# Kernel optimization log

Hardware: AMD Instinct MI355X
Metric: run time of the kernel (lower is better)

The kernel has to match this reference:

```python
import jax, jax.numpy as jnp
import numpy as np

C = 768; H = 12; D = C // H; R = 8; SCALE = 0.5; EPS = 1e-12
NEG = -1e9

def _lin(x, W, b):
    return x @ W + b

def _ln(x, g, b):
    m = jnp.mean(x, axis=-1, keepdims=True)
    v = jnp.mean((x - m) ** 2, axis=-1, keepdims=True)
    return (x - m) * jax.lax.rsqrt(v + EPS) * g + b

def setup_inputs() -> dict:
    key = jax.random.key(0)
    ks = jax.random.split(key, 16)
    B, T, K = 8, 512, 4
    s = 0.02
    inp = {
        'x': jax.random.normal(ks[0], (B, T, C), jnp.float32),
        'mask': jnp.ones((B, T), jnp.int32),
        'neighbour_rep': jax.random.normal(ks[1], (B, T - 1, K, C), jnp.float32),
        'Wq': jax.random.normal(ks[2], (C, C), jnp.float32) * s,
        'bq': jnp.zeros((C,), jnp.float32),
        'Wk': jax.random.normal(ks[3], (C, C), jnp.float32) * s,
        'bk': jnp.zeros((C,), jnp.float32),
        'Wv': jax.random.normal(ks[4], (C, C), jnp.float32) * s,
        'bv': jnp.zeros((C,), jnp.float32),
        'Wp': jax.random.normal(ks[5], (C, C), jnp.float32) * s,
        'bp': jnp.zeros((C,), jnp.float32),
        'Wd': jax.random.normal(ks[6], (C, R), jnp.float32) * s,
        'bd': jnp.zeros((R,), jnp.float32),
        'Wu': jax.random.normal(ks[7], (R, C), jnp.float32) * s,
        'bu': jnp.zeros((C,), jnp.float32),
        'ln_g': jnp.ones((C,), jnp.float32),
        'ln_b': jnp.zeros((C,), jnp.float32),
    }
    return inp

def _softmax_stable(att):
    # manual max-sub-exp-sum softmax, matching stable_softmax
    att = att - jnp.max(att, axis=-1, keepdims=True)
    att = jnp.exp(att)
    return att / jnp.sum(att, axis=-1, keepdims=True)

def _heads(t, n_tok):
    B = t.shape[0]
    return t.reshape(B, n_tok, H, D)

def reference(x, mask, neighbour_rep, Wq, bq, Wk, bk, Wv, bv, Wp, bp, Wd, bd, Wu, bu, ln_g, ln_b):
    B, T, _ = x.shape
    inv = 1.0 / jnp.sqrt(jnp.float32(D))
    mvalid = (mask != 0)[:, None, None, :]  # [B,1,1,T]

    # ---- self attention: queries are x[:,1:], keys/values over full seq ----
    q = _heads(_lin(x[:, 1:], Wq, bq), T - 1)      # [B,T-1,H,D]
    k = _heads(_lin(x, Wk, bk), T)                 # [B,T,H,D]
    v = _heads(_lin(x, Wv, bv), T)
    att = jnp.einsum('bqhd,bkhd->bhqk', q, k) * inv
    att = jnp.where(mvalid, att, NEG)
    att = _softmax_stable(att)
    y_self = jnp.einsum('bhqk,bkhd->bqhd', att, v).reshape(B, T - 1, C)
    y_self = _lin(y_self, Wp, bp)

    # ---- cls attention: single query (token 0), low-rank key projection ----
    qc = _heads(_lin(x[:, :1], Wq, bq), 1)                         # [B,1,H,D]
    kc = _heads(_lin(_lin(x, Wd, bd), Wu, bu), T)                  # [B,T,H,D]
    attc = jnp.einsum('bqhd,bkhd->bhqk', qc, kc) * inv
    attc = jnp.where(mvalid, attc, NEG)
    attc = _softmax_stable(attc)
    y_cls = jnp.einsum('bhqk,bkhd->bqhd', attc, v).reshape(B, 1, C)
    y_cls = _lin(y_cls, Wp, bp)

    # ---- neighbour attention over small candidate set per token ----
    cand = jnp.concatenate([x[:, 1:, None, :], neighbour_rep], axis=2)  # [B,T-1,Kc,C]
    Kc = cand.shape[2]
    qn = _lin(cand, Wq, bq).reshape(B, T - 1, Kc, H, D)
    kn = _lin(_lin(cand, Wd, bd), Wu, bu).reshape(B, T - 1, Kc, H, D)
    vn = _lin(cand, Wv, bv).reshape(B, T - 1, Kc, H, D)
    attn = jnp.einsum('btihd,btjhd->bthij', qn, kn) * inv
    attn = _softmax_stable(attn)
    out = jnp.einsum('bthij,btjhd->btihd', attn, vn).reshape(B, T - 1, Kc, C)
    out = _lin(out, Wp, bp)
    y_neigh = out[:, :, 0, :]
    neigh_tmp = out[:, :, 1:, :]

    y = SCALE * y_neigh + (1.0 - SCALE) * y_self
    neighbour_out = _ln(neigh_tmp + neighbour_rep, ln_g, ln_b)
    y = jnp.concatenate([y_cls, y], axis=1)
    y = _ln(y + x, ln_g, ln_b)
    return y, neighbour_out
```

## Files before the change

### kernel.cpp

```cpp
#include <hip/hip_runtime.h>
#include <math.h>

#define C_    768
#define H_    12
#define D_    64
#define B_    8
#define T_    512
#define TM1   511
#define R_    8
#define KN_   4
#define KC5   5
#define SCALE_ 0.5f
#define EPS_  1e-12f
#define NEG_  -1000000000.0f
#define INV_  0.125f
#define LDQ   2432
#define QPOFF 2304
#define LDVQ  896
#define NT_   4096
#define NRR_  16352

typedef __bf16 bf16_t;
typedef __bf16 bf16x4_t __attribute__((ext_vector_type(4)));
typedef __bf16 bf16x8_t __attribute__((ext_vector_type(8)));
typedef float  f32x4_t  __attribute__((ext_vector_type(4)));
typedef const void __attribute__((address_space(1)))* gas_t;
typedef void       __attribute__((address_space(3)))* las_t;

__device__ __forceinline__ void gl_lds16(const bf16_t* g, bf16_t* l) {
  __builtin_amdgcn_global_load_lds((gas_t)g, (las_t)l, 16, 0, 0);
}

struct GemmDesc {
  const bf16_t* A; int lda;
  const bf16_t* Bt;
  const float* bias;
  bf16_t* Cbf; int ldc;
  bf16_t* Ctr; int trcol0; int mode;
  int M, K, N, gx, nwg;
};

__global__ __launch_bounds__(256) void prep(
    const float* __restrict__ x, const float* __restrict__ nrep,
    const float* __restrict__ Wq, const float* __restrict__ Wk,
    const float* __restrict__ Wv, const float* __restrict__ Wp,
    const float* __restrict__ Wd, const float* __restrict__ Wu,
    const float* __restrict__ bq, const float* __restrict__ bk,
    const float* __restrict__ bv, const float* __restrict__ bu,
    const float* __restrict__ bp,
    bf16_t* __restrict__ xbf, bf16_t* __restrict__ nrbf,
    bf16_t* __restrict__ Wbig, bf16_t* __restrict__ Wtp,
    bf16_t* __restrict__ Wvbf,
    float* __restrict__ WdT, float* __restrict__ bbig,
    float* __restrict__ zb768)
{
  __shared__ float tile[32][33];
  const int bid = blockIdx.x, tid = threadIdx.x;
  if (bid < 1024) {
    const long n = (long)NT_ * C_;
    for (long i = ((long)bid * 256 + tid) * 4; i < n; i += (long)1024 * 256 * 4) {
      float4 v = *(const float4*)(x + i);
      bf16x4_t o = {(bf16_t)v.x, (bf16_t)v.y, (bf16_t)v.z, (bf16_t)v.w};
      *(bf16x4_t*)(xbf + i) = o;
    }
  } else if (bid < 3072) {
    const long n = (long)NRR_ * C_;
    for (long i = ((long)(bid - 1024) * 256 + tid) * 4; i < n;
         i += (long)2048 * 256 * 4) {
      float4 v = *(const float4*)(nrep + i);
      bf16x4_t o = {(bf16_t)v.x, (bf16_t)v.y, (bf16_t)v.z, (bf16_t)v.w};
      *(bf16x4_t*)(nrbf + i) = o;
    }
  } else if (bid < 5376) {
    int sub = bid - 3072;
    const int which = sub / 576; sub %= 576;
    if (which == 2) {
      const long i = ((long)sub * 256 + tid) * 4;
      float4 v = *(const float4*)(Wv + i);
      bf16x4_t o = {(bf16_t)v.x, (bf16_t)v.y, (bf16_t)v.z, (bf16_t)v.w};
      *(bf16x4_t*)(Wvbf + i) = o;
    } else {
      const float* W = which == 0 ? Wq : which == 1 ? Wk : Wp;
      bf16_t* Wt = (which == 3) ? Wtp : Wbig + (size_t)which * C_ * C_;
      const int n0 = (sub % 24) * 32, k0 = (sub / 24) * 32;
      const int tx = tid & 31, ty = tid >> 5;
      #pragma unroll
      for (int r = ty; r < 32; r += 8)
        tile[r][tx] = W[(size_t)(k0 + r) * C_ + n0 + tx];
      __syncthreads();
      #pragma unroll
      for (int r = ty; r < 32; r += 8)
        Wt[(size_t)(n0 + r) * C_ + k0 + tx] = (bf16_t)tile[tx][r];
    }
  } else if (bid < 5760) {
    const int idx = (bid - 5376) * 256 + tid;
    const int n = idx / C_, k = idx % C_;
    const int h = n / 10, r = n % 10;
    float s = 0.f;
    if (h < H_ && r < 9) {
      if (r < 8) {
        #pragma unroll 8
        for (int j = 0; j < 64; ++j)
          s += Wu[r * C_ + h * 64 + j] * Wq[(size_t)k * C_ + h * 64 + j];
      } else {
        #pragma unroll 8
        for (int j = 0; j < 64; ++j)
          s += bu[h * 64 + j] * Wq[(size_t)k * C_ + h * 64 + j];
      }
    }
    Wbig[(size_t)(QPOFF + n) * C_ + k] = (bf16_t)s;
  } else if (bid < 5784) {
    const int idx = (bid - 5760) * 256 + tid;
    if (idx < R_ * C_) {
      const int r = idx / C_, k = idx % C_;
      WdT[idx] = Wd[(size_t)k * R_ + r];
    }
  } else {
    const int i = (bid - 5784) * 256 + tid;
    if (i < LDQ) {
      float v;
      if (i < 768) v = bq[i];
      else if (i < 1536) v = bk[i - 768];
      else if (i < 2304) {
        const int n = i - 1536;
        float s = bp[n];
        for (int m = 0; m < C_; ++m) s += bv[m] * Wp[(size_t)m * C_ + n];
        v = s;
      } else {
        const int n = i - QPOFF, h = n / 10, r = n % 10;
        v = 0.f;
        if (h < H_ && r < 9) {
          if (r < 8) {
            float s = 0.f;
            for (int j = 0; j < 64; ++j) s += bq[h * 64 + j] * Wu[r * C_ + h * 64 + j];
            v = s;
          } else {
            float s = 0.f;
            for (int j = 0; j < 64; ++j) s += bq[h * 64 + j] * bu[h * 64 + j];
            v = s;
          }
        }
      }
      bbig[i] = v;
    } else if (i < LDQ + 768) {
      zb768[i - LDQ] = 0.f;
    }
  }
}

__device__ __forceinline__ void gemm_body(const GemmDesc& d, int bid0, char* pool)
{
  bf16_t* As = (bf16_t*)pool;
  bf16_t* Bs = (bf16_t*)(pool + 16384);
  bf16_t* Cs = (bf16_t*)pool;

  int lid = bid0;
  {
    const int nwg = d.nwg;
    const int q0 = nwg >> 3, r0 = nwg & 7;
    const int xcd = lid & 7, idx = lid >> 3;
    lid = (xcd < r0 ? xcd * (q0 + 1) : r0 * (q0 + 1) + (xcd - r0) * q0) + idx;
  }
  const int row0 = (lid / d.gx) * 128;
  const int col0 = (lid % d.gx) * 128;

  const int tid = threadIdx.x;
  const int lane = tid & 63;
  const int wv = tid >> 6;
  const int wr = (wv >> 1) * 64;
  const int wc = (wv & 1) * 64;

  const int srl = wv * 8 + (lane >> 3);
  const int scol = 8 * ((lane & 7) ^ (srl & 7));

  const bf16_t* gA[4];
  const bf16_t* gB[4];
  #pragma unroll
  for (int i = 0; i < 4; ++i) {
    int ar = row0 + i * 32 + srl; if (ar > d.M - 1) ar = d.M - 1;
    gA[i] = d.A + (size_t)ar * d.lda + scol;
    gB[i] = d.Bt + (size_t)(col0 + i * 32 + srl) * d.K + scol;
  }

  f32x4_t acc[4][4];
  #pragma unroll
  for (int i = 0; i < 4; ++i)
    #pragma unroll
    for (int j = 0; j < 4; ++j) acc[i][j] = (f32x4_t){0.f, 0.f, 0.f, 0.f};

  const int fm = lane & 15;
  const int g = lane >> 4;
  const int f7 = fm & 7;

  for (int k0 = 0; k0 < d.K; k0 += 64) {
    #pragma unroll
    for (int i = 0; i < 4; ++i)
      gl_lds16(gA[i] + k0, As + i * 2048 + wv * 512);
    #pragma unroll
    for (int i = 0; i < 4; ++i)
      gl_lds16(gB[i] + k0, Bs + i * 2048 + wv * 512);
    __syncthreads();
    #pragma unroll
    for (int h = 0; h < 2; ++h) {
      const int sl = 8 * (((h << 2) + g) ^ f7);
      bf16x8_t af[4], bfr[4];
      #pragma unroll
      for (int mi = 0; mi < 4; ++mi)
        af[mi] = *(const bf16x8_t*)(As + (wr + mi * 16 + fm) * 64 + sl);
      #pragma unroll
      for (int ni = 0; ni < 4; ++ni)
        bfr[ni] = *(const bf16x8_t*)(Bs + (wc + ni * 16 + fm) * 64 + sl);
      __builtin_amdgcn_s_setprio(1);
      #pragma unroll
      for (int mi = 0; mi < 4; ++mi)
        #pragma unroll
        for (int ni = 0; ni < 4; ++ni)
          acc[mi][ni] = __builtin_amdgcn_mfma_f32_16x16x32_bf16(af[mi], bfr[ni],
                                                                acc[mi][ni], 0, 0, 0);
      __builtin_amdgcn_s_setprio(0);
    }
    __syncthreads();
  }

  const int r4 = (lane >> 4) * 4;

  if (d.mode & 2) {
    #pragma unroll
    for (int ni = 0; ni < 4; ++ni) {
      const int col = col0 + wc + ni * 16 + fm;
      if ((unsigned)(col - d.trcol0) < 768u) {
        const int vcol = col - d.trcol0;
        const float bv = d.bias[col];
        #pragma unroll
        for (int mi = 0; mi < 4; ++mi) {
          const int rb = row0 + wr + mi * 16 + r4;
          bf16x4_t o4 = {(bf16_t)(acc[mi][ni][0] + bv), (bf16_t)(acc[mi][ni][1] + bv),
                         (bf16_t)(acc[mi][ni][2] + bv), (bf16_t)(acc[mi][ni][3] + bv)};
          size_t idx = ((size_t)(rb >> 9) * H_ + (size_t)(vcol >> 6)) * ((size_t)D_ * T_)
                     + (size_t)(vcol & 63) * T_ + (size_t)(rb & 511);
          *(bf16x4_t*)(d.Ctr + idx) = o4;
        }
      }
    }
  }

  #pragma unroll
  for (int p = 0; p < 2; ++p) {
    if (wr == p * 64) {
      #pragma unroll
      for (int ni = 0; ni < 4; ++ni) {
        const int col = wc + ni * 16 + fm;
        const float bv = d.bias[col0 + col];
        #pragma unroll
        for (int mi = 0; mi < 4; ++mi) {
          const int lrow = mi * 16 + r4;
          #pragma unroll
          for (int r = 0; r < 4; ++r)
            Cs[(lrow + r) * 136 + col] = (bf16_t)(acc[mi][ni][r] + bv);
        }
      }
    }
    __syncthreads();
    const int rrow = tid >> 2;
    const int cc = (tid & 3) * 32;
    const int grow = row0 + p * 64 + rrow;
    if ((d.mode & 1) && grow < d.M) {
      bf16_t* gp = d.Cbf + (size_t)grow * d.ldc + col0 + cc;
      const bf16_t* lp = Cs + rrow * 136 + cc;
      #pragma unroll
      for (int j = 0; j < 4; ++j)
        *(bf16x8_t*)(gp + j * 8) = *(const bf16x8_t*)(lp + j * 8);
    }
    __syncthreads();
  }
}

__device__ __forceinline__ void gemv8w_body(
    const bf16_t* __restrict__ A, const float* __restrict__ WdT,
    const float* __restrict__ bd, float* __restrict__ out, int M, int bid)
{
  const int w = (int)threadIdx.x >> 6, lane = (int)threadIdx.x & 63;
  const int row0 = bid * 16 + w * 4;
  #pragma unroll
  for (int rr = 0; rr < 4; ++rr) {
    const int row = row0 + rr;
    if (row >= M) return;
    const bf16_t* ar = A + (size_t)row * C_ + lane * 12;
    float xv[12];
    #pragma unroll
    for (int c = 0; c < 3; ++c) {
      bf16x4_t v = *(const bf16x4_t*)(ar + c * 4);
      #pragma unroll
      for (int j = 0; j < 4; ++j) xv[c * 4 + j] = (float)v[j];
    }
    float acc[8];
    #pragma unroll
    for (int r = 0; r < 8; ++r) {
      const float* wr = WdT + r * C_ + lane * 12;
      float4 w0 = *(const float4*)(wr);
      float4 w1 = *(const float4*)(wr + 4);
      float4 w2 = *(const float4*)(wr + 8);
      acc[r] = xv[0]*w0.x + xv[1]*w0.y + xv[2]*w0.z + xv[3]*w0.w
             + xv[4]*w1.x + xv[5]*w1.y + xv[6]*w1.z + xv[7]*w1.w
             + xv[8]*w2.x + xv[9]*w2.y + xv[10]*w2.z + xv[11]*w2.w;
    }
    #pragma unroll
    for (int off = 32; off > 0; off >>= 1) {
      #pragma unroll
      for (int r = 0; r < 8; ++r) acc[r] += __shfl_xor(acc[r], off);
    }
    if (lane == 0) {
      #pragma unroll
      for (int r = 0; r < 8; ++r)
        out[(size_t)row * R_ + r] = acc[r] + bd[r];
    }
  }
}

__global__ __launch_bounds__(256) void mega1(
    GemmDesc d0, int n0, GemmDesc d1, int n1,
    const bf16_t* Ag1, const bf16_t* Ag2,
    const float* WdT, const float* bd,
    float* o1, int M1, int ng1, float* o2, int M2)
{
  __shared__ __align__(16) char pool[32768];
  int bid = blockIdx.x;
  if (bid < n0) { gemm_body(d0, bid, pool); return; }
  bid -= n0;
  if (bid < n1) { gemm_body(d1, bid, pool); return; }
  bid -= n1;
  if (bid < ng1) { gemv8w_body(Ag1, WdT, bd, o1, M1, bid); return; }
  bid -= ng1;
  gemv8w_body(Ag2, WdT, bd, o2, M2, bid);
}

__global__ __launch_bounds__(256) void gemm_mfma_k(GemmDesc d) {
  __shared__ __align__(16) char pool[32768];
  gemm_body(d, blockIdx.x, pool);
}

__device__ void attn_body(
    const bf16_t* __restrict__ QKVc, const bf16_t* __restrict__ Vtg,
    const int* __restrict__ mask, bf16_t* __restrict__ yout,
    char* pool, int bid)
{
  bf16_t* Ks   = (bf16_t*)pool;
  bf16_t* Vs   = (bf16_t*)(pool + 8192);
  bf16_t* Pl   = (bf16_t*)(pool + 16384);
  float* fac_s = (float*)(pool + 24576);
  float* l_s   = (float*)(pool + 24832);
  int*   msk_s = (int*)(pool + 25088);

  const int qt0 = (bid & 7) * 64;
  const int h = (bid >> 3) % H_;
  const int b = bid / 96;
  const int tid = threadIdx.x;
  const int lane = tid & 63;
  const int w = tid >> 6;
  const int lq = lane & 15;
  const int g = lane >> 4;

  const int qi_frag = qt0 + w * 16 + lq;
  const int qtok = (qi_frag < TM1 ? qi_frag : TM1 - 1) + 1;
  bf16x8_t qf[2];
  {
    const bf16_t* qp = QKVc + ((size_t)(b * T_) + qtok) * LDQ + h * D_ + 8 * g;
    qf[0] = *(const bf16x8_t*)qp;
    qf[1] = *(const bf16x8_t*)(qp + 32);
  }

  const bf16_t* kbase = QKVc + (size_t)(b * T_) * LDQ + 768 + h * D_;
  const bf16_t* vbase = Vtg + ((size_t)(b * H_) + h) * ((size_t)D_ * T_);

  f32x4_t o[4];
  #pragma unroll
  for (int i = 0; i < 4; ++i) o[i] = (f32x4_t){0.f, 0.f, 0.f, 0.f};
  float m = -INFINITY, l = 0.f;

  for (int kt = 0; kt < T_; kt += 64) {
    #pragma unroll
    for (int i = 0; i < 2; ++i) {
      const int tp = tid + i * 256;
      const int kr = tp >> 3;
      const int sl = tp & 7;
      const int ss = sl ^ (kr & 7);
      gl_lds16(kbase + (size_t)(kt + kr) * LDQ + 8 * ss,
               Ks + (size_t)(i * 4 + w) * 512);
      gl_lds16(vbase + (size_t)kr * T_ + kt + 8 * ss,
               Vs + (size_t)(i * 4 + w) * 512);
    }
    if (tid < 64) msk_s[tid] = mask[b * T_ + kt + tid];
    __syncthreads();

    f32x4_t st[4];
    __builtin_amdgcn_s_setprio(1);
    #pragma unroll
    for (int t = 0; t < 4; ++t) {
      st[t] = (f32x4_t){0.f, 0.f, 0.f, 0.f};
      const int kk = t * 16 + lq;
      const bf16_t* krow = Ks + kk * 64;
      bf16x8_t kf0 = *(const bf16x8_t*)(krow + 8 * ((g)     ^ (kk & 7)));
      bf16x8_t kf1 = *(const bf16x8_t*)(krow + 8 * ((4 + g) ^ (kk & 7)));
      st[t] = __builtin_amdgcn_mfma_f32_16x16x32_bf16(kf0, qf[0], st[t], 0, 0, 0);
      st[t] = __builtin_amdgcn_mfma_f32_16x16x32_bf16(kf1, qf[1], st[t], 0, 0, 0);
    }
    __builtin_amdgcn_s_setprio(0);

    float p[16];
    float mt = -INFINITY;
    #pragma unroll
    for (int t = 0; t < 4; ++t) {
      const int4 mk = *(const int4*)&msk_s[t * 16 + 4 * g];
      p[4*t+0] = mk.x ? st[t][0] * INV_ : NEG_;
      p[4*t+1] = mk.y ? st[t][1] * INV_ : NEG_;
      p[4*t+2] = mk.z ? st[t][2] * INV_ : NEG_;
      p[4*t+3] = mk.w ? st[t][3] * INV_ : NEG_;
      mt = fmaxf(mt, fmaxf(fmaxf(p[4*t], p[4*t+1]), fmaxf(p[4*t+2], p[4*t+3])));
    }
    mt = fmaxf(mt, __shfl_xor(mt, 16));
    mt = fmaxf(mt, __shfl_xor(mt, 32));
    const float mnew = fmaxf(m, mt);
    const float fac = __expf(m - mnew);
    float ps = 0.f;
    #pragma unroll
    for (int i = 0; i < 16; ++i) { p[i] = __expf(p[i] - mnew); ps += p[i]; }
    ps += __shfl_xor(ps, 16);
    ps += __shfl_xor(ps, 32);
    l = l * fac + ps;
    m = mnew;
    if (lane < 16) fac_s[w * 16 + lane] = fac;

    bf16_t* prow = Pl + w * 1024 + lq * 64;
    #pragma unroll
    for (int t = 0; t < 4; ++t) {
      bf16x4_t pb = {(bf16_t)p[4*t], (bf16_t)p[4*t+1],
                     (bf16_t)p[4*t+2], (bf16_t)p[4*t+3]};
      *(bf16x4_t*)(prow + 8 * ((2*t + (g >> 1)) ^ (lq & 7)) + 4 * (g & 1)) = pb;
    }
    bf16x8_t pa0 = *(const bf16x8_t*)(prow + 8 * ((g)     ^ (lq & 7)));
    bf16x8_t pa1 = *(const bf16x8_t*)(prow + 8 * ((4 + g) ^ (lq & 7)));

    const float4 fc = *(const float4*)&fac_s[w * 16 + 4 * g];
    __builtin_amdgcn_s_setprio(1);
    #pragma unroll
    for (int db = 0; db < 4; ++db) {
      const int dr = db * 16 + lq;
      const bf16_t* vrow = Vs + dr * 64;
      bf16x8_t vf0 = *(const bf16x8_t*)(vrow + 8 * ((g)     ^ (dr & 7)));
      bf16x8_t vf1 = *(const bf16x8_t*)(vrow + 8 * ((4 + g) ^ (dr & 7)));
      o[db][0] *= fc.x; o[db][1] *= fc.y; o[db][2] *= fc.z; o[db][3] *= fc.w;
      o[db] = __builtin_amdgcn_mfma_f32_16x16x32_bf16(pa0, vf0, o[db], 0, 0, 0);
      o[db] = __builtin_amdgcn_mfma_f32_16x16x32_bf16(pa1, vf1, o[db], 0, 0, 0);
    }
    __builtin_amdgcn_s_setprio(0);
    __syncthreads();
  }

  if (lane < 16) l_s[w * 16 + lane] = l;
  const float4 lv = *(const float4*)&l_s[w * 16 + 4 * g];
  const float rl0 = 1.f / lv.x, rl1 = 1.f / lv.y;
  const float rl2 = 1.f / lv.z, rl3 = 1.f / lv.w;
  const int qr0 = qt0 + w * 16 + 4 * g;
  #pragma unroll
  for (int db = 0; db < 4; ++db) {
    const int col = h * D_ + db * 16 + lq;
    bf16_t* yp = yout + ((size_t)(b * TM1) + qr0) * C_ + col;
    if (qr0 + 0 < TM1) yp[0 * (size_t)C_] = (bf16_t)(o[db][0] * rl0);
    if (qr0 + 1 < TM1) yp[1 * (size_t)C_] = (bf16_t)(o[db][1] * rl1);
    if (qr0 + 2 < TM1) yp[2 * (size_t)C_] = (bf16_t)(o[db][2] * rl2);
    if (qr0 + 3 < TM1) yp[3 * (size_t)C_] = (bf16_t)(o[db][3] * rl3);
  }
}

__device__ void cls_body(
    const bf16_t* __restrict__ QKVc, const float* __restrict__ t1,
    const int* __restrict__ mask, float* __restrict__ ycp,
    char* pool, int cbid)
{
  float* Vs   = (float*)pool;
  float* Ps   = (float*)(pool + 16640);
  float* qp_s = (float*)(pool + 16960);

  const int b = cbid / H_, h = cbid % H_;
  const int tid = threadIdx.x;
  const int lane = tid & 63;

  if (tid < 9)
    qp_s[tid] = (float)QKVc[(size_t)(b * T_) * LDQ + QPOFF + h * 10 + tid];
  __syncthreads();

  float m = -INFINITY, l = 0.f, acc = 0.f, mnew = 0.f;
  for (int kt = 0; kt < T_; kt += 64) {
    for (int rr = tid >> 6; rr < 64; rr += 4)
      Vs[rr * 65 + lane] =
          (float)QKVc[((size_t)(b * T_) + kt + rr) * LDQ + 1536 + h * D_ + lane];
    __syncthreads();
    if (tid < 64) {
      const float* t1r = t1 + ((size_t)(b * T_) + kt + tid) * R_;
      float sc = qp_s[8];
      #pragma unroll
      for (int r = 0; r < 8; ++r) sc += qp_s[r] * t1r[r];
      sc *= INV_;
      if (!mask[b * T_ + kt + tid]) sc = NEG_;
      float mt = sc;
      #pragma unroll
      for (int off = 32; off > 0; off >>= 1) mt = fmaxf(mt, __shfl_xor(mt, off));
      mnew = fmaxf(m, mt);
      float e = __expf(sc - mnew);
      float ssum = e;
      #pragma unroll
      for (int off = 32; off > 0; off >>= 1) ssum += __shfl_xor(ssum, off);
      float fac = __expf(m - mnew);
      acc *= fac;
      l = l * fac + ssum;
      Ps[tid] = e;
    }
    __syncthreads();
    if (tid < 64) {
      #pragma unroll
      for (int j = 0; j < 64; ++j) acc += Ps[j] * Vs[j * 65 + tid];
      m = mnew;
    }
    __syncthreads();
  }
  if (tid < 64) ycp[(size_t)b * C_ + h * D_ + tid] = acc / l;
}

__global__ __launch_bounds__(256) void attn_cls(
    const bf16_t* __restrict__ QKVc, const bf16_t* __restrict__ Vtg,
    const int* __restrict__ mask, bf16_t* __restrict__ yout,
    const float* __restrict__ t1, float* __restrict__ ycp)
{
  __shared__ __align__(16) char pool[25344];
  const int bid = blockIdx.x;
  if (bid < 768) attn_body(QKVc, Vtg, mask, yout, pool, bid);
  else           cls_body(QKVc, t1, mask, ycp, pool, bid - 768);
}

__global__ __launch_bounds__(256) void neigh_attn(
    const bf16_t* __restrict__ QKVc, const float* __restrict__ t1,
    const bf16_t* __restrict__ vqn, const float* __restrict__ t2,
    const bf16_t* __restrict__ ysp, int b0, bf16_t* __restrict__ poutn)
{
  __shared__ float vs[KC5 * C_];
  __shared__ float qp_s[KC5][128];
  __shared__ float t2_s[KC5][8];
  __shared__ float Ps[H_ * 25];

  const int tid = threadIdx.x;
  const int bt = blockIdx.x;
  const int bb = bt / TM1, t = bt % TM1;
  const int b = b0 + bb;
  const size_t tok = (size_t)(b * T_) + t + 1;
  const size_t nrow = ((size_t)(bb * TM1) + t) * KN_;

  for (int idx = tid; idx < KC5 * 96; idx += 256) {
    int i = idx / 96, d8 = (idx % 96) * 8;
    const bf16_t* vp = (i == 0) ? QKVc + tok * LDQ + 1536 + d8
                                : vqn + (nrow + i - 1) * LDVQ + d8;
    bf16x8_t vv = *(const bf16x8_t*)vp;
    #pragma unroll
    for (int j = 0; j < 8; ++j) vs[i * C_ + d8 + j] = (float)vv[j];
  }
  for (int idx = tid; idx < KC5 * 16; idx += 256) {
    int i = idx / 16, c8 = (idx % 16) * 8;
    const bf16_t* qpp = (i == 0) ? QKVc + tok * LDQ + QPOFF + c8
                                 : vqn + (nrow + i - 1) * LDVQ + 768 + c8;
    bf16x8_t qv = *(const bf16x8_t*)qpp;
    #pragma unroll
    for (int j = 0; j < 8; ++j) qp_s[i][c8 + j] = (float)qv[j];
  }
  if (tid < KC5 * 8) {
    int i = tid / 8, r = tid & 7;
    t2_s[i][r] = (i == 0) ? t1[tok * R_ + r] : t2[(nrow + i - 1) * R_ + r];
  }
  __syncthreads();

  if (tid < H_ * KC5) {
    int h = tid / KC5, i = tid % KC5;
    float sc[KC5];
    #pragma unroll
    for (int j = 0; j < KC5; ++j) {
      float s = qp_s[i][h * 10 + 8];
      #pragma unroll
      for (int r = 0; r < 8; ++r) s += qp_s[i][h * 10 + r] * t2_s[j][r];
      sc[j] = s * INV_;
    }
    float mt = sc[0];
    #pragma unroll
    for (int j = 1; j < KC5; ++j) mt = fmaxf(mt, sc[j]);
    float e[KC5], ssum = 0.f;
    #pragma unroll
    for (int j = 0; j < KC5; ++j) { e[j] = __expf(sc[j] - mt); ssum += e[j]; }
    float rs = 1.f / ssum;
    #pragma unroll
    for (int j = 0; j < KC5; ++j) Ps[h * 25 + i * KC5 + j] = e[j] * rs;
  }
  __syncthreads();

  const bf16_t* ysrow = ysp + ((size_t)(b * TM1) + t) * C_;
  for (int idx = tid; idx < KC5 * C_; idx += 256) {
    int i = idx / C_, c = idx % C_;
    int h = c / D_;
    float sum = 0.f;
    #pragma unroll
    for (int j = 0; j < KC5; ++j)
      sum += Ps[h * 25 + i * KC5 + j] * vs[j * C_ + c];
    if (i == 0) sum = SCALE_ * sum + (1.f - SCALE_) * (float)ysrow[c];
    poutn[(((size_t)(bb * TM1) + t) * KC5 + i) * C_ + c] = (bf16_t)sum;
  }
}

__device__ __forceinline__ void block_reduce2(float& s, float& ss, float* red) {
  #pragma unroll
  for (int off = 32; off > 0; off >>= 1) {
    s += __shfl_down(s, off);
    ss += __shfl_down(ss, off);
  }
  int wid = threadIdx.x >> 6;
  if ((threadIdx.x & 63) == 0) { red[wid * 2] = s; red[wid * 2 + 1] = ss; }
  __syncthreads();
  s  = red[0] + red[2] + red[4] + red[6];
  ss = red[1] + red[3] + red[5] + red[7];
}

__device__ __forceinline__ void ln_row(const float vals[3], float s, float ss,
                                       const float* __restrict__ g,
                                       const float* __restrict__ bb,
                                       float* __restrict__ orow, float* red) {
  block_reduce2(s, ss, red);
  float mean = s * (1.f / (float)C_);
  float var = ss * (1.f / (float)C_) - mean * mean;
  var = fmaxf(var, 0.f);
  float rs = rsqrtf(var + EPS_);
  #pragma unroll
  for (int ii = 0; ii < 3; ++ii) {
    int c = threadIdx.x + ii * 256;
    orow[c] = (vals[ii] - mean) * rs * g[c] + bb[c];
  }
}

__global__ __launch_bounds__(256) void combine_all(
    const bf16_t* __restrict__ poutnb, const float* __restrict__ x,
    const float* __restrict__ g, const float* __restrict__ bln,
    int b0, float* __restrict__ dout, float* __restrict__ dout1,
    const bf16_t* __restrict__ nrcbf, int nMain,
    const float* __restrict__ ycp)
{
  __shared__ float red[8];
  int bid = blockIdx.x;
  float vals[3], s = 0.f, ss = 0.f;
  if (bid < nMain) {
    const int bbb = bid / TM1, t = bid % TM1;
    const int b = b0 + bbb;
    const bf16_t* pn = poutnb + (((size_t)(bbb * TM1) + t) * KC5 + 0) * C_;
    const float* xr = x + ((size_t)(b * T_) + t + 1) * C_;
    float* orow = dout + ((size_t)(b * T_) + t + 1) * C_;
    #pragma unroll
    for (int ii = 0; ii < 3; ++ii) {
      int c = threadIdx.x + ii * 256;
      float v = (float)pn[c] + xr[c];
      vals[ii] = v; s += v; ss += v * v;
    }
    ln_row(vals, s, ss, g, bln, orow, red);
    return;
  }
  bid -= nMain;
  if (bid < nMain * KN_) {
    const int i1 = bid % KN_;
    const int bt = bid / KN_;
    const int bbb = bt / TM1, t = bt % TM1;
    const int b = b0 + bbb;
    const bf16_t* pn = poutnb + ((size_t)bt * KC5 + 1 + i1) * C_;
    const bf16_t* nr = nrcbf + ((size_t)bt * KN_ + i1) * C_;
    float* orow = dout1 + (((size_t)(b * TM1) + t) * KN_ + i1) * C_;
    #pragma unroll
    for (int ii = 0; ii < 3; ++ii) {
      int c = threadIdx.x + ii * 256;
      float v = (float)pn[c] + (float)nr[c];
      vals[ii] = v; s += v; ss += v * v;
    }
    ln_row(vals, s, ss, g, bln, orow, red);
    return;
  }
  bid -= nMain * KN_;
  const int b = bid;
  const float* yc = ycp + (size_t)b * C_;
  const float* xr = x + (size_t)(b * T_) * C_;
  float* orow = dout + (size_t)(b * T_) * C_;
  #pragma unroll
  for (int ii = 0; ii < 3; ++ii) {
    int c = threadIdx.x + ii * 256;
    float v = yc[c] + xr[c];
    vals[ii] = v; s += v; ss += v * v;
  }
  ln_row(vals, s, ss, g, bln, orow, red);
}

extern "C" void kernel_launch(void* const* d_in, const int* in_sizes, int n_in,
                              void* d_out, int out_size, void* d_ws, size_t ws_size,
                              hipStream_t stream) {
  (void)in_sizes; (void)n_in; (void)out_size;
  const float* x    = (const float*)d_in[0];
  const int*   mask = (const int*)d_in[1];
  const float* nrep = (const float*)d_in[2];
  const float* Wq = (const float*)d_in[3];  const float* bq = (const float*)d_in[4];
  const float* Wk = (const float*)d_in[5];  const float* bk = (const float*)d_in[6];
  const float* Wv = (const float*)d_in[7];  const float* bv = (const float*)d_in[8];
  const float* Wp = (const float*)d_in[9];  const float* bp = (const float*)d_in[10];
  const float* Wd = (const float*)d_in[11]; const float* bd = (const float*)d_in[12];
  const float* Wu = (const float*)d_in[13]; const float* bu = (const float*)d_in[14];
  const float* lng = (const float*)d_in[15];
  const float* lnb = (const float*)d_in[16];
  float* dout = (float*)d_out;
  const size_t OUT1 = (size_t)B_ * T_ * C_;

  char* ws = (char*)d_ws;
  size_t off = 0;
  auto alloc = [&](size_t bytes) -> void* {
    void* p = ws + off; off += (bytes + 255) & ~(size_t)255; return p;
  };
  const size_t NT = (size_t)NT_;
  const size_t NR = (size_t)NRR_;
  const size_t YSROWS = (size_t)B_ * TM1;

  bf16_t* xbf   = (bf16_t*)alloc(NT * C_ * 2);
  bf16_t* nrbf  = (bf16_t*)alloc(NR * C_ * 2);
  bf16_t* Wbig  = (bf16_t*)alloc((size_t)LDQ * C_ * 2);
  bf16_t* Wtp   = (bf16_t*)alloc((size_t)C_ * C_ * 2);
  bf16_t* Wvbf  = (bf16_t*)alloc((size_t)C_ * C_ * 2);
  float*  WdT   = (float*)alloc((size_t)R_ * C_ * 4);
  float*  bbig  = (float*)alloc(LDQ * 4);
  float*  zb768 = (float*)alloc(768 * 4);
  bf16_t* QKVc  = (bf16_t*)alloc(NT * LDQ * 2);
  bf16_t* Vtg   = (bf16_t*)alloc(NT * C_ * 2);
  float*  t1    = (float*)alloc(NT * R_ * 4);
  bf16_t* ysp   = (bf16_t*)alloc(YSROWS * C_ * 2);
  float*  ycp   = (float*)alloc((size_t)B_ * C_ * 4);
  const size_t fixed = off;
  const size_t perb = (size_t)TM1 * KN_ * LDVQ * 2
                    + (size_t)TM1 * KN_ * R_ * 4
                    + (size_t)TM1 * KC5 * C_ * 2 + 4 * 256;
  int nb = 1;
  for (int cand : {8, 4, 2, 1}) {
    if (fixed + perb * (size_t)cand <= ws_size) { nb = cand; break; }
  }
  bf16_t* poutnb = (bf16_t*)alloc((size_t)nb * TM1 * KC5 * C_ * 2);
  bf16_t* vqn  = (bf16_t*)alloc((size_t)nb * TM1 * KN_ * LDVQ * 2);
  float*  t2   = (float*)alloc((size_t)nb * TM1 * KN_ * R_ * 4);

  dim3 blk(256);

  prep<<<5797, blk, 0, stream>>>(x, nrep, Wq, Wk, Wv, Wp, Wd, Wu,
                                 bq, bk, bv, bu, bp,
                                 xbf, nrbf, Wbig, Wtp, Wvbf, WdT, bbig, zb768);

  GemmDesc dwvp;
  dwvp.A = Wtp; dwvp.lda = C_; dwvp.Bt = Wvbf; dwvp.bias = zb768;
  dwvp.Cbf = Wbig + (size_t)1536 * C_; dwvp.ldc = C_;
  dwvp.Ctr = nullptr; dwvp.trcol0 = 0; dwvp.mode = 1;
  dwvp.M = C_; dwvp.K = C_; dwvp.N = C_; dwvp.gx = 6; dwvp.nwg = 36;
  gemm_mfma_k<<<36, blk, 0, stream>>>(dwvp);

  GemmDesc dqkv;
  dqkv.A = xbf; dqkv.lda = C_; dqkv.Bt = Wbig; dqkv.bias = bbig;
  dqkv.Cbf = QKVc; dqkv.ldc = LDQ; dqkv.Ctr = Vtg; dqkv.trcol0 = 1536;
  dqkv.mode = 3; dqkv.M = (int)NT; dqkv.K = C_; dqkv.N = LDQ;
  dqkv.gx = LDQ / 128; dqkv.nwg = (LDQ / 128) * 32;

  bool first = true;
  for (int b0 = 0; b0 < B_; b0 += nb) {
    const int Mn = nb * TM1 * KN_;
    const bf16_t* nrcbf = nrbf + (size_t)b0 * TM1 * KN_ * C_;

    GemmDesc dvqn;
    dvqn.A = nrcbf; dvqn.lda = C_; dvqn.Bt = Wbig + (size_t)1536 * C_;
    dvqn.bias = bbig + 1536; dvqn.Cbf = vqn; dvqn.ldc = LDVQ;
    dvqn.Ctr = nullptr; dvqn.trcol0 = 0; dvqn.mode = 1;
    dvqn.M = Mn; dvqn.K = C_; dvqn.N = LDVQ;
    dvqn.gx = LDVQ / 128; dvqn.nwg = (LDVQ / 128) * ((Mn + 127) / 128);

    const int n0 = first ? dqkv.nwg : 0;
    const int M1 = first ? (int)NT : 0;
    const int ng1 = first ? (int)((NT + 15) / 16) : 0;
    const int ng2 = (Mn + 15) / 16;

    mega1<<<n0 + dvqn.nwg + ng1 + ng2, blk, 0, stream>>>(
        dqkv, n0, dvqn, dvqn.nwg, xbf, nrcbf, WdT, bd, t1, M1, ng1, t2, Mn);

    if (first) {
      attn_cls<<<768 + 96, blk, 0, stream>>>(QKVc, Vtg, mask, ysp, t1, ycp);
    }

    neigh_attn<<<nb * TM1, blk, 0, stream>>>(QKVc, t1, vqn, t2, ysp, b0, poutnb);

    combine_all<<<nb * TM1 * (1 + KN_) + (first ? 8 : 0), blk, 0, stream>>>(
        poutnb, x, lng, lnb, b0, dout, dout + OUT1, nrcbf, nb * TM1, ycp);

    first = false;
  }
}
```

Before: 238.0 us.

## Double-buffer GEMM LDS tiles with BK=32 and prefetch next tile

Result: no change. 236.8 us (-0.5%).

```diff
diff --git a/kernel.cpp b/kernel.cpp
--- a/kernel.cpp
+++ b/kernel.cpp
@@ -29,6 +29,10 @@
 
 __device__ __forceinline__ void gl_lds16(const bf16_t* g, bf16_t* l) {
   __builtin_amdgcn_global_load_lds((gas_t)g, (las_t)l, 16, 0, 0);
+}
+
+__device__ __forceinline__ int swz(int row, int g) {
+  return row * 32 + (((g ^ (row >> 1)) & 3) << 3);
 }
 
 struct GemmDesc {
@@ -150,8 +154,6 @@
 
 __device__ __forceinline__ void gemm_body(const GemmDesc& d, int bid0, char* pool)
 {
-  bf16_t* As = (bf16_t*)pool;
-  bf16_t* Bs = (bf16_t*)(pool + 16384);
   bf16_t* Cs = (bf16_t*)pool;
 
   int lid = bid0;
@@ -169,18 +171,18 @@
   const int wv = tid >> 6;
   const int wr = (wv >> 1) * 64;
   const int wc = (wv & 1) * 64;
-
-  const int srl = wv * 8 + (lane >> 3);
-  const int scol = 8 * ((lane & 7) ^ (srl & 7));
-
-  const bf16_t* gA[4];
-  const bf16_t* gB[4];
-  #pragma unroll
-  for (int i = 0; i < 4; ++i) {
-    int ar = row0 + i * 32 + srl; if (ar > d.M - 1) ar = d.M - 1;
-    gA[i] = d.A + (size_t)ar * d.lda + scol;
-    gB[i] = d.Bt + (size_t)(col0 + i * 32 + srl) * d.K + scol;
-  }
+  const int wvo = wv * 512;
+
+  const int sr = tid >> 2;
+  const int ssl = (tid & 3) ^ ((sr >> 1) & 3);
+  const int sk = ssl * 8;
+
+  int ra0 = row0 + sr;       if (ra0 > d.M - 1) ra0 = d.M - 1;
+  int ra1 = row0 + 64 + sr;  if (ra1 > d.M - 1) ra1 = d.M - 1;
+  const bf16_t* ga0 = d.A + (size_t)ra0 * d.lda + sk;
+  const bf16_t* ga1 = d.A + (size_t)ra1 * d.lda + sk;
+  const bf16_t* gb0 = d.Bt + (size_t)(col0 + sr) * d.K + sk;
+  const bf16_t* gb1 = d.Bt + (size_t)(col0 + 64 + sr) * d.K + sk;
 
   f32x4_t acc[4][4];
   #pragma unroll
@@ -190,26 +192,38 @@
 
   const int fm = lane & 15;
   const int g = lane >> 4;
-  const int f7 = fm & 7;
-
-  for (int k0 = 0; k0 < d.K; k0 += 64) {
-    #pragma unroll
-    for (int i = 0; i < 4; ++i)
-      gl_lds16(gA[i] + k0, As + i * 2048 + wv * 512);
-    #pragma unroll
-    for (int i = 0; i < 4; ++i)
-      gl_lds16(gB[i] + k0, Bs + i * 2048 + wv * 512);
-    __syncthreads();
-    #pragma unroll
-    for (int h = 0; h < 2; ++h) {
-      const int sl = 8 * (((h << 2) + g) ^ f7);
+
+  {
+    bf16_t* a0 = (bf16_t*)pool;
+    bf16_t* b0 = (bf16_t*)(pool + 8192);
+    gl_lds16(ga0, a0 + wvo);
+    gl_lds16(ga1, a0 + 2048 + wvo);
+    gl_lds16(gb0, b0 + wvo);
+    gl_lds16(gb1, b0 + 2048 + wvo);
+  }
+  __syncthreads();
+
+  unsigned cur = 0;
+  for (int k0 = 32; k0 < d.K; k0 += 32) {
+    {
+      char* nb = pool + ((cur ^ 1u) << 14);
+      bf16_t* na = (bf16_t*)nb;
+      bf16_t* nbb = (bf16_t*)(nb + 8192);
+      gl_lds16(ga0 + k0, na + wvo);
+      gl_lds16(ga1 + k0, na + 2048 + wvo);
+      gl_lds16(gb0 + k0, nbb + wvo);
+      gl_lds16(gb1 + k0, nbb + 2048 + wvo);
+    }
+    {
+      const bf16_t* cA = (const bf16_t*)(pool + (cur << 14));
+      const bf16_t* cB = (const bf16_t*)(pool + (cur << 14) + 8192);
       bf16x8_t af[4], bfr[4];
       #pragma unroll
       for (int mi = 0; mi < 4; ++mi)
-        af[mi] = *(const bf16x8_t*)(As + (wr + mi * 16 + fm) * 64 + sl);
+        af[mi] = *(const bf16x8_t*)(cA + swz(wr + mi * 16 + fm, g));
       #pragma unroll
       for (int ni = 0; ni < 4; ++ni)
-        bfr[ni] = *(const bf16x8_t*)(Bs + (wc + ni * 16 + fm) * 64 + sl);
+        bfr[ni] = *(const bf16x8_t*)(cB + swz(wc + ni * 16 + fm, g));
       __builtin_amdgcn_s_setprio(1);
       #pragma unroll
       for (int mi = 0; mi < 4; ++mi)
@@ -220,7 +234,28 @@
       __builtin_amdgcn_s_setprio(0);
     }
     __syncthreads();
-  }
+    cur ^= 1u;
+  }
+  {
+    const bf16_t* cA = (const bf16_t*)(pool + (cur << 14));
+    const bf16_t* cB = (const bf16_t*)(pool + (cur << 14) + 8192);
+    bf16x8_t af[4], bfr[4];
+    #pragma unroll
+    for (int mi = 0; mi < 4; ++mi)
+      af[mi] = *(const bf16x8_t*)(cA + swz(wr + mi * 16 + fm, g));
+    #pragma unroll
+    for (int ni = 0; ni < 4; ++ni)
+      bfr[ni] = *(const bf16x8_t*)(cB + swz(wc + ni * 16 + fm, g));
+    __builtin_amdgcn_s_setprio(1);
+    #pragma unroll
+    for (int mi = 0; mi < 4; ++mi)
+      #pragma unroll
+      for (int ni = 0; ni < 4; ++ni)
+        acc[mi][ni] = __builtin_amdgcn_mfma_f32_16x16x32_bf16(af[mi], bfr[ni],
+                                                              acc[mi][ni], 0, 0, 0);
+    __builtin_amdgcn_s_setprio(0);
+  }
+  __syncthreads();
 
   const int r4 = (lane >> 4) * 4;
 
```
